# Kernel optimization log

Hardware: AMD Instinct MI355X
Metric: run time of the kernel (lower is better)

Reference implementation:

```python
import jax, jax.numpy as jnp
import numpy as np

B, D = 16384, 1280      # batch, EfficientNet-b0 feature dim (model._fc.in_features)
C1, C2, C3 = 8, 6, 4    # fanout per tree level: 8 roots, 6 children each, 4 leaves each


def setup_inputs() -> dict:
    key = jax.random.key(0)
    ks = jax.random.split(key, 7)
    sc = 0.02
    x = jax.random.normal(ks[0], (B, D), dtype=jnp.float32)
    # root classifier: self.final = Linear(1280 -> n[0]=8)
    W_final = jax.random.normal(ks[1], (D, C1), dtype=jnp.float32) * sc
    b_final = jnp.zeros((C1,), dtype=jnp.float32)
    # level-1 node linears: Linear(1281 -> 6); split into feature part Wp and upper-scalar column wu
    Wp1 = jax.random.normal(ks[2], (C1, D, C2), dtype=jnp.float32) * sc
    wu1 = jax.random.normal(ks[3], (C1, C2), dtype=jnp.float32) * sc
    b1 = jnp.zeros((C1, C2), dtype=jnp.float32)
    # level-2 node linears: Linear(1281 -> 4)
    Wp2 = jax.random.normal(ks[4], (C1, C2, D, C3), dtype=jnp.float32) * sc
    wu2 = jax.random.normal(ks[5], (C1, C2, C3), dtype=jnp.float32) * sc
    b2 = jnp.zeros((C1, C2, C3), dtype=jnp.float32)
    return {"x": x, "W_final": W_final, "b_final": b_final,
            "Wp1": Wp1, "wu1": wu1, "b1": b1,
            "Wp2": Wp2, "wu2": wu2, "b2": b2}


def reference(x, W_final, b_final, Wp1, wu1, b1, Wp2, wu2, b2):
    # penultimate = x.clone().detach()
    pen = jax.lax.stop_gradient(x)                      # (B, D)
    # root: raw final-linear outputs (NO softmax at root in the torch code)
    u1 = x @ W_final + b_final                          # (B, C1) == upper for level-1 nodes
    # level-1 nodes: line = softmax(Linear([pen, upper_scalar]))
    # Linear([pen, u]) == pen @ Wp + u * wu + b  (batched over all 8 nodes in one GEMM)
    logits1 = jnp.einsum('bd,idc->bic', pen, Wp1) + u1[:, :, None] * wu1[None] + b1[None]
    p1 = jax.nn.softmax(logits1, axis=-1)               # (B, C1, C2)
    u2 = p1 * u1[:, :, None]                            # upper for level-2 nodes
    # level-2 nodes
    logits2 = jnp.einsum('bd,ijdc->bijc', pen, Wp2) + u2[..., None] * wu2[None] + b2[None]
    p2 = jax.nn.softmax(logits2, axis=-1)               # (B, C1, C2, C3)
    u3 = p2 * u2[..., None]                             # upper for leaf nodes
    # output: for each node (sorted by path length, then lexicographic path),
    # the last column of xdict[node] == upper[node]. Row-major reshape matches
    # the sorted key order for single-char labels.
    return jnp.concatenate([u1, u2.reshape(B, C1 * C2), u3.reshape(B, C1 * C2 * C3)], axis=1)
```

## Files before the change

kernel.cpp:

```cpp
#include <hip/hip_runtime.h>
#include <stdint.h>
#include <stddef.h>

#define D_FEAT 1280
#define N_PAD  256
#define N_OUT  248
#define BM     32
#define BK     64
#define K_ITERS 20
#define W_TILE_BYTES (N_PAD * BK * 2)

typedef float f32x4 __attribute__((ext_vector_type(4)));
typedef short s16x8 __attribute__((ext_vector_type(8)));
typedef unsigned int u32x4 __attribute__((ext_vector_type(4)));

__device__ __forceinline__ unsigned int cvt_pk(float a, float b) {
  unsigned int r;
  asm("v_cvt_pk_bf16_f32 %0, %1, %2" : "=v"(r) : "v"(a), "v"(b));
  return r;
}

__device__ __forceinline__ void gload16(const void* g, void* l) {
  __builtin_amdgcn_global_load_lds(
      (const __attribute__((address_space(1))) void*)g,
      (__attribute__((address_space(3))) void*)l, 16, 0, 0);
}

__global__ __launch_bounds__(256) void pack_w_kernel(
    const float* __restrict__ Wf, const float* __restrict__ Wp1,
    const float* __restrict__ Wp2, unsigned short* __restrict__ out) {
  int chunk = blockIdx.x * 256 + threadIdx.x;
  int s_phys = chunk & 7;
  int n = (chunk >> 3) & 255;
  int kt = chunk >> 11;
  int s_log = s_phys ^ (n & 7);
  int d0 = kt * BK + s_log * 8;
  float v[8];
#pragma unroll
  for (int e = 0; e < 8; ++e) v[e] = 0.0f;
  if (n < 8) {
#pragma unroll
    for (int e = 0; e < 8; ++e) v[e] = Wf[(d0 + e) * 8 + n];
  } else if (n < 56) {
    int m = n - 8;
    const float* base = Wp1 + (size_t)(m / 6) * D_FEAT * 6 + (m % 6);
#pragma unroll
    for (int e = 0; e < 8; ++e) v[e] = base[(d0 + e) * 6];
  } else if (n < 248) {
    int m = n - 56;
    const float* base = Wp2 + ((size_t)(m / 24) * 6 + ((m % 24) >> 2)) * D_FEAT * 4 + (m & 3);
#pragma unroll
    for (int e = 0; e < 8; ++e) v[e] = base[(d0 + e) * 4];
  }
  union { u32x4 u; s16x8 s; } pk;
#pragma unroll
  for (int h = 0; h < 4; ++h) pk.u[h] = cvt_pk(v[2 * h], v[2 * h + 1]);
  *(s16x8*)(out + (size_t)chunk * 8) = pk.s;
}

__global__ __launch_bounds__(256, 2) void tree_head_kernel(
    const float* __restrict__ x, const unsigned short* __restrict__ Wb,
    const float* __restrict__ b_final, const float* __restrict__ wu1,
    const float* __restrict__ b1, const float* __restrict__ wu2,
    const float* __restrict__ b2, float* __restrict__ out) {
  __shared__ __align__(16) char smem[73728];
  char* Ab0 = smem;
  char* Ab1 = smem + 4096;
  char* Bb0 = smem + 8192;
  char* Bb1 = smem + 40960;

  const int tid  = threadIdx.x;
  const int lane = tid & 63;
  const int wave = tid >> 6;
  const int l15  = lane & 15;
  const int lh   = lane >> 4;
  const int row0 = blockIdx.x * BM;

  f32x4 acc[2][4];
#pragma unroll
  for (int m = 0; m < 2; ++m)
#pragma unroll
    for (int n = 0; n < 4; ++n)
#pragma unroll
      for (int j = 0; j < 4; ++j) acc[m][n][j] = 0.0f;

  const int arow = tid >> 3;
  const int aslot = tid & 7;
  const char* aptr = (const char*)x + ((size_t)(row0 + arow) * D_FEAT + aslot * 8) * 4;
  const int awoff = arow * 128 + ((aslot ^ (arow & 7)) << 4);
  const char* bsrc = (const char*)Wb + wave * 1024 + lane * 16;
  const int bdst = wave * 1024;

  f32x4 ra[3][2];

#define STAGEB(kt_, dB_) do {                                                 \
    _Pragma("unroll")                                                         \
    for (int j_ = 0; j_ < 8; ++j_)                                            \
      gload16(bsrc + (size_t)(kt_) * W_TILE_BYTES + j_ * 4096,                \
              (dB_) + bdst + j_ * 4096);                                      \
  } while (0)

#define LOADA(kt_, ri_) do {                                                  \
    ra[ri_][0] = *(const f32x4*)(aptr + (kt_) * 256);                         \
    ra[ri_][1] = *(const f32x4*)(aptr + (kt_) * 256 + 16);                    \
  } while (0)

#define WRITEA(ri_, dA_) do {                                                 \
    union { u32x4 u; s16x8 s; } pk_;                                          \
    pk_.u[0] = cvt_pk(ra[ri_][0][0], ra[ri_][0][1]);                          \
    pk_.u[1] = cvt_pk(ra[ri_][0][2], ra[ri_][0][3]);                          \
    pk_.u[2] = cvt_pk(ra[ri_][1][0], ra[ri_][1][1]);                          \
    pk_.u[3] = cvt_pk(ra[ri_][1][2], ra[ri_][1][3]);                          \
    *(s16x8*)((dA_) + awoff) = pk_.s;                                         \
  } while (0)

#define COMPUTE(cA_, cB_) do {                                                \
    s16x8 fr[2][2];                                                           \
    _Pragma("unroll")                                                         \
    for (int m_ = 0; m_ < 2; ++m_) {                                          \
      int rl_ = m_ * 16 + l15;                                                \
      _Pragma("unroll")                                                       \
      for (int ks_ = 0; ks_ < 2; ++ks_) {                                     \
        int sl_ = ks_ * 4 + lh;                                               \
        fr[m_][ks_] = *(const s16x8*)((cA_) + rl_ * 128 +                     \
                                      ((sl_ ^ (rl_ & 7)) << 4));              \
      }                                                                       \
    }                                                                         \
    _Pragma("unroll")                                                         \
    for (int ks_ = 0; ks_ < 2; ++ks_) {                                       \
      int sl_ = ks_ * 4 + lh;                                                 \
      _Pragma("unroll")                                                       \
      for (int nf_ = 0; nf_ < 4; ++nf_) {                                     \
        int n_ = wave * 64 + nf_ * 16 + l15;                                  \
        s16x8 b_ = *(const s16x8*)((cB_) + n_ * 128 + ((sl_ ^ (n_ & 7)) << 4));\
        acc[0][nf_] = __builtin_amdgcn_mfma_f32_16x16x32_bf16(fr[0][ks_], b_, acc[0][nf_], 0, 0, 0); \
        acc[1][nf_] = __builtin_amdgcn_mfma_f32_16x16x32_bf16(fr[1][ks_], b_, acc[1][nf_], 0, 0, 0); \
      }                                                                       \
    }                                                                         \
  } while (0)

#define ITER(vm_, cA_, cB_, wA_, sB_, skt_, lakt_, ls_, ws_) do {             \
    asm volatile("s_waitcnt vmcnt(" #vm_ ") lgkmcnt(0)" ::: "memory");        \
    __builtin_amdgcn_sched_barrier(0);                                        \
    __builtin_amdgcn_s_barrier();                                             \
    __builtin_amdgcn_sched_barrier(0);                                        \
    STAGEB(skt_, sB_);                                                        \
    LOADA(lakt_, ls_);                                                        \
    __builtin_amdgcn_sched_barrier(0);                                        \
    WRITEA(ws_, wA_);                                                         \
    COMPUTE(cA_, cB_);                                                        \
  } while (0)

  STAGEB(0, Bb0);
  LOADA(0, 0);
  LOADA(1, 1);
  LOADA(2, 2);
  __builtin_amdgcn_sched_barrier(0);
  asm volatile("s_waitcnt vmcnt(4)" ::: "memory");
  __builtin_amdgcn_sched_barrier(0);
  WRITEA(0, Ab0);

  for (int t = 0; t < 2; ++t) {
    ITER(2, Ab0, Bb0, Ab1, Bb1, 6 * t + 1, 6 * t + 3, 0, 1);
    ITER(2, Ab1, Bb1, Ab0, Bb0, 6 * t + 2, 6 * t + 4, 1, 2);
    ITER(2, Ab0, Bb0, Ab1, Bb1, 6 * t + 3, 6 * t + 5, 2, 0);
    ITER(2, Ab1, Bb1, Ab0, Bb0, 6 * t + 4, 6 * t + 6, 0, 1);
    ITER(2, Ab0, Bb0, Ab1, Bb1, 6 * t + 5, 6 * t + 7, 1, 2);
    ITER(2, Ab1, Bb1, Ab0, Bb0, 6 * t + 6, 6 * t + 8, 2, 0);
  }
  ITER(2, Ab0, Bb0, Ab1, Bb1, 13, 15, 0, 1);
  ITER(2, Ab1, Bb1, Ab0, Bb0, 14, 16, 1, 2);
  ITER(2, Ab0, Bb0, Ab1, Bb1, 15, 17, 2, 0);
  ITER(2, Ab1, Bb1, Ab0, Bb0, 16, 18, 0, 1);
  ITER(2, Ab0, Bb0, Ab1, Bb1, 17, 19, 1, 2);

  asm volatile("s_waitcnt vmcnt(2) lgkmcnt(0)" ::: "memory");
  __builtin_amdgcn_sched_barrier(0);
  __builtin_amdgcn_s_barrier();
  __builtin_amdgcn_sched_barrier(0);
  STAGEB(18, Bb0);
  __builtin_amdgcn_sched_barrier(0);
  WRITEA(0, Ab0);
  COMPUTE(Ab1, Bb1);

  asm volatile("s_waitcnt vmcnt(0) lgkmcnt(0)" ::: "memory");
  __builtin_amdgcn_sched_barrier(0);
  __builtin_amdgcn_s_barrier();
  __builtin_amdgcn_sched_barrier(0);
  STAGEB(19, Bb1);
  __builtin_amdgcn_sched_barrier(0);
  WRITEA(1, Ab1);
  COMPUTE(Ab0, Bb0);

  asm volatile("s_waitcnt vmcnt(0) lgkmcnt(0)" ::: "memory");
  __builtin_amdgcn_sched_barrier(0);
  __builtin_amdgcn_s_barrier();
  __builtin_amdgcn_sched_barrier(0);
  COMPUTE(Ab1, Bb1);

  __syncthreads();

  float* Ls = (float*)smem;
#pragma unroll
  for (int m = 0; m < 2; ++m)
#pragma unroll
    for (int nf = 0; nf < 4; ++nf) {
      int col = wave * 64 + nf * 16 + l15;
      if (col < N_OUT) {
        int rbase = m * 16 + (lh << 2);
#pragma unroll
        for (int i = 0; i < 4; ++i) Ls[col * 33 + rbase + i] = acc[m][nf][i];
      }
    }
  __syncthreads();

  const int p = tid & 7;
  const int r = tid >> 3;
  float* orow = out + (size_t)(row0 + r) * N_OUT;

  float ui = Ls[p * 33 + r] + b_final[p];
  orow[p] = ui;

  float lg[6];
  float mx = -1e30f;
#pragma unroll
  for (int c = 0; c < 6; ++c) {
    lg[c] = Ls[(8 + p * 6 + c) * 33 + r] + ui * wu1[p * 6 + c] + b1[p * 6 + c];
    mx = fmaxf(mx, lg[c]);
  }
  float s = 0.0f;
#pragma unroll
  for (int c = 0; c < 6; ++c) { lg[c] = __expf(lg[c] - mx); s += lg[c]; }
  float sc = ui / s;
  float u2v[6];
#pragma unroll
  for (int c = 0; c < 6; ++c) {
    u2v[c] = lg[c] * sc;
    orow[8 + p * 6 + c] = u2v[c];
  }

#pragma unroll
  for (int j = 0; j < 6; ++j) {
    int g = p * 6 + j;
    float ug = u2v[j];
    float l2[4];
    float m2 = -1e30f;
#pragma unroll
    for (int c = 0; c < 4; ++c) {
      l2[c] = Ls[(56 + g * 4 + c) * 33 + r] + ug * wu2[g * 4 + c] + b2[g * 4 + c];
      m2 = fmaxf(m2, l2[c]);
    }
    float s2 = 0.0f;
#pragma unroll
    for (int c = 0; c < 4; ++c) { l2[c] = __expf(l2[c] - m2); s2 += l2[c]; }
    float sc2 = ug / s2;
    f32x4 o;
#pragma unroll
    for (int c = 0; c < 4; ++c) o[c] = l2[c] * sc2;
    *(f32x4*)(orow + 56 + g * 4) = o;
  }
#undef STAGEB
#undef LOADA
#undef WRITEA
#undef COMPUTE
#undef ITER
}

extern "C" void kernel_launch(void* const* d_in, const int* in_sizes, int n_in,
                              void* d_out, int out_size, void* d_ws, size_t ws_size,
                              hipStream_t stream) {
  const float* x   = (const float*)d_in[0];
  const float* Wf  = (const float*)d_in[1];
  const float* bf  = (const float*)d_in[2];
  const float* Wp1 = (const float*)d_in[3];
  const float* wu1 = (const float*)d_in[4];
  const float* b1  = (const float*)d_in[5];
  const float* Wp2 = (const float*)d_in[6];
  const float* wu2 = (const float*)d_in[7];
  const float* b2  = (const float*)d_in[8];
  float* out = (float*)d_out;
  unsigned short* Wb = (unsigned short*)d_ws;

  pack_w_kernel<<<160, 256, 0, stream>>>(Wf, Wp1, Wp2, Wb);
  tree_head_kernel<<<16384 / BM, 256, 0, stream>>>(x, Wb, bf, wu1, b1, wu2, b2, out);
}
```

Baseline: 37.92 us.

## Load A fragments directly to registers and give each wave private B buffers

```diff
diff --git a/kernel.cpp b/kernel.cpp
--- a/kernel.cpp
+++ b/kernel.cpp
@@ -63,11 +63,7 @@
     const float* __restrict__ b_final, const float* __restrict__ wu1,
     const float* __restrict__ b1, const float* __restrict__ wu2,
     const float* __restrict__ b2, float* __restrict__ out) {
-  __shared__ __align__(16) char smem[73728];
-  char* Ab0 = smem;
-  char* Ab1 = smem + 4096;
-  char* Bb0 = smem + 8192;
-  char* Bb1 = smem + 40960;
+  __shared__ __align__(16) char smem[65536];
 
   const int tid  = threadIdx.x;
   const int lane = tid & 63;
@@ -76,6 +72,8 @@
   const int lh   = lane >> 4;
   const int row0 = blockIdx.x * BM;
 
+  char* Bme = smem + wave * 16384;
+
   f32x4 acc[2][4];
 #pragma unroll
   for (int m = 0; m < 2; ++m)
@@ -84,119 +82,88 @@
 #pragma unroll
       for (int j = 0; j < 4; ++j) acc[m][n][j] = 0.0f;
 
-  const int arow = tid >> 3;
-  const int aslot = tid & 7;
-  const char* aptr = (const char*)x + ((size_t)(row0 + arow) * D_FEAT + aslot * 8) * 4;
-  const int awoff = arow * 128 + ((aslot ^ (arow & 7)) << 4);
-  const char* bsrc = (const char*)Wb + wave * 1024 + lane * 16;
-  const int bdst = wave * 1024;
-
-  f32x4 ra[3][2];
-
-#define STAGEB(kt_, dB_) do {                                                 \
+  const char* abase = (const char*)x
+      + ((size_t)(row0 + l15) * D_FEAT + lh * 8) * 4;
+  const char* bsrc = (const char*)Wb + wave * 8192 + lane * 16;
+
+  f32x4 ra[3][8];
+
+#define STAGEB(kt_, db_) do {                                                 \
     _Pragma("unroll")                                                         \
     for (int j_ = 0; j_ < 8; ++j_)                                            \
-      gload16(bsrc + (size_t)(kt_) * W_TILE_BYTES + j_ * 4096,                \
-              (dB_) + bdst + j_ * 4096);                                      \
-  } while (0)
-
-#define LOADA(kt_, ri_) do {                                                  \
-    ra[ri_][0] = *(const f32x4*)(aptr + (kt_) * 256);                         \
-    ra[ri_][1] = *(const f32x4*)(aptr + (kt_) * 256 + 16);                    \
-  } while (0)
-
-#define WRITEA(ri_, dA_) do {                                                 \
-    union { u32x4 u; s16x8 s; } pk_;                                          \
-    pk_.u[0] = cvt_pk(ra[ri_][0][0], ra[ri_][0][1]);                          \
-    pk_.u[1] = cvt_pk(ra[ri_][0][2], ra[ri_][0][3]);                          \
-    pk_.u[2] = cvt_pk(ra[ri_][1][0], ra[ri_][1][1]);                          \
-    pk_.u[3] = cvt_pk(ra[ri_][1][2], ra[ri_][1][3]);                          \
-    *(s16x8*)((dA_) + awoff) = pk_.s;                                         \
-  } while (0)
-
-#define COMPUTE(cA_, cB_) do {                                                \
+      gload16(bsrc + (size_t)(kt_) * W_TILE_BYTES + j_ * 1024,                \
+              Bme + (db_) * 8192 + j_ * 1024);                                \
+  } while (0)
+
+#define LOADA(kt_, s_) do {                                                   \
+    _Pragma("unroll")                                                         \
+    for (int m_ = 0; m_ < 2; ++m_)                                            \
+      _Pragma("unroll")                                                       \
+      for (int ks_ = 0; ks_ < 2; ++ks_)                                       \
+        _Pragma("unroll")                                                     \
+        for (int h_ = 0; h_ < 2; ++h_)                                        \
+          ra[s_][m_ * 4 + ks_ * 2 + h_] = *(const f32x4*)(                    \
+              abase + m_ * (16 * D_FEAT * 4) + (kt_) * 256 + ks_ * 128 + h_ * 16); \
+  } while (0)
+
+#define COMPUTE(s_, db_) do {                                                 \
     s16x8 fr[2][2];                                                           \
     _Pragma("unroll")                                                         \
-    for (int m_ = 0; m_ < 2; ++m_) {                                          \
-      int rl_ = m_ * 16 + l15;                                                \
+    for (int m_ = 0; m_ < 2; ++m_)                                            \
       _Pragma("unroll")                                                       \
       for (int ks_ = 0; ks_ < 2; ++ks_) {                                     \
-        int sl_ = ks_ * 4 + lh;                                               \
-        fr[m_][ks_] = *(const s16x8*)((cA_) + rl_ * 128 +                     \
-                                      ((sl_ ^ (rl_ & 7)) << 4));              \
+        union { u32x4 u; s16x8 s; } pk_;                                      \
+        f32x4 f0_ = ra[s_][m_ * 4 + ks_ * 2];                                 \
+        f32x4 f1_ = ra[s_][m_ * 4 + ks_ * 2 + 1];                             \
+        pk_.u[0] = cvt_pk(f0_[0], f0_[1]); pk_.u[1] = cvt_pk(f0_[2], f0_[3]); \
+        pk_.u[2] = cvt_pk(f1_[0], f1_[1]); pk_.u[3] = cvt_pk(f1_[2], f1_[3]); \
+        fr[m_][ks_] = pk_.s;                                                  \
       }                                                                       \
-    }                                                                         \
+    __builtin_amdgcn_s_setprio(1);                                            \
     _Pragma("unroll")                                                         \
     for (int ks_ = 0; ks_ < 2; ++ks_) {                                       \
       int sl_ = ks_ * 4 + lh;                                                 \
       _Pragma("unroll")                                                       \
       for (int nf_ = 0; nf_ < 4; ++nf_) {                                     \
-        int n_ = wave * 64 + nf_ * 16 + l15;                                  \
-        s16x8 b_ = *(const s16x8*)((cB_) + n_ * 128 + ((sl_ ^ (n_ & 7)) << 4));\
+        int nl_ = nf_ * 16 + l15;                                             \
+        s16x8 b_ = *(const s16x8*)(Bme + (db_) * 8192 + nl_ * 128 +           \
+                                   ((sl_ ^ (nl_ & 7)) << 4));                 \
         acc[0][nf_] = __builtin_amdgcn_mfma_f32_16x16x32_bf16(fr[0][ks_], b_, acc[0][nf_], 0, 0, 0); \
         acc[1][nf_] = __builtin_amdgcn_mfma_f32_16x16x32_bf16(fr[1][ks_], b_, acc[1][nf_], 0, 0, 0); \
       }                                                                       \
     }                                                                         \
-  } while (0)
-
-#define ITER(vm_, cA_, cB_, wA_, sB_, skt_, lakt_, ls_, ws_) do {             \
-    asm volatile("s_waitcnt vmcnt(" #vm_ ") lgkmcnt(0)" ::: "memory");        \
+    __builtin_amdgcn_s_setprio(0);                                            \
+  } while (0)
+
+#define ITER(kt_, db_, dbn_, sc_, sn_) do {                                   \
+    asm volatile("s_waitcnt vmcnt(8)" ::: "memory");                          \
     __builtin_amdgcn_sched_barrier(0);                                        \
-    __builtin_amdgcn_s_barrier();                                             \
+    STAGEB((kt_) + 1, dbn_);                                                  \
+    LOADA((kt_) + 2, sn_);                                                    \
     __builtin_amdgcn_sched_barrier(0);                                        \
-    STAGEB(skt_, sB_);                                                        \
-    LOADA(lakt_, ls_);                                                        \
-    __builtin_amdgcn_sched_barrier(0);                                        \
-    WRITEA(ws_, wA_);                                                         \
-    COMPUTE(cA_, cB_);                                                        \
-  } while (0)
-
-  STAGEB(0, Bb0);
+    COMPUTE(sc_, db_);                                                        \
+  } while (0)
+
+  STAGEB(0, 0);
   LOADA(0, 0);
   LOADA(1, 1);
-  LOADA(2, 2);
+
+  for (int t = 0; t < 3; ++t) {
+    ITER(6 * t + 0, 0, 1, 0, 2);
+    ITER(6 * t + 1, 1, 0, 1, 0);
+    ITER(6 * t + 2, 0, 1, 2, 1);
+    ITER(6 * t + 3, 1, 0, 0, 2);
+    ITER(6 * t + 4, 0, 1, 1, 0);
+    ITER(6 * t + 5, 1, 0, 2, 1);
+  }
+  asm volatile("s_waitcnt vmcnt(8)" ::: "memory");
   __builtin_amdgcn_sched_barrier(0);
-  asm volatile("s_waitcnt vmcnt(4)" ::: "memory");
+  STAGEB(19, 1);
   __builtin_amdgcn_sched_barrier(0);
-  WRITEA(0, Ab0);
-
-  for (int t = 0; t < 2; ++t) {
-    ITER(2, Ab0, Bb0, Ab1, Bb1, 6 * t + 1, 6 * t + 3, 0, 1);
-    ITER(2, Ab1, Bb1, Ab0, Bb0, 6 * t + 2, 6 * t + 4, 1, 2);
-    ITER(2, Ab0, Bb0, Ab1, Bb1, 6 * t + 3, 6 * t + 5, 2, 0);
-    ITER(2, Ab1, Bb1, Ab0, Bb0, 6 * t + 4, 6 * t + 6, 0, 1);
-    ITER(2, Ab0, Bb0, Ab1, Bb1, 6 * t + 5, 6 * t + 7, 1, 2);
-    ITER(2, Ab1, Bb1, Ab0, Bb0, 6 * t + 6, 6 * t + 8, 2, 0);
-  }
-  ITER(2, Ab0, Bb0, Ab1, Bb1, 13, 15, 0, 1);
-  ITER(2, Ab1, Bb1, Ab0, Bb0, 14, 16, 1, 2);
-  ITER(2, Ab0, Bb0, Ab1, Bb1, 15, 17, 2, 0);
-  ITER(2, Ab1, Bb1, Ab0, Bb0, 16, 18, 0, 1);
-  ITER(2, Ab0, Bb0, Ab1, Bb1, 17, 19, 1, 2);
-
-  asm volatile("s_waitcnt vmcnt(2) lgkmcnt(0)" ::: "memory");
+  COMPUTE(0, 0);
+  asm volatile("s_waitcnt vmcnt(0)" ::: "memory");
   __builtin_amdgcn_sched_barrier(0);
-  __builtin_amdgcn_s_barrier();
-  __builtin_amdgcn_sched_barrier(0);
-  STAGEB(18, Bb0);
-  __builtin_amdgcn_sched_barrier(0);
-  WRITEA(0, Ab0);
-  COMPUTE(Ab1, Bb1);
-
-  asm volatile("s_waitcnt vmcnt(0) lgkmcnt(0)" ::: "memory");
-  __builtin_amdgcn_sched_barrier(0);
-  __builtin_amdgcn_s_barrier();
-  __builtin_amdgcn_sched_barrier(0);
-  STAGEB(19, Bb1);
-  __builtin_amdgcn_sched_barrier(0);
-  WRITEA(1, Ab1);
-  COMPUTE(Ab0, Bb0);
-
-  asm volatile("s_waitcnt vmcnt(0) lgkmcnt(0)" ::: "memory");
-  __builtin_amdgcn_sched_barrier(0);
-  __builtin_amdgcn_s_barrier();
-  __builtin_amdgcn_sched_barrier(0);
-  COMPUTE(Ab1, Bb1);
+  COMPUTE(1, 1);
 
   __syncthreads();
 
@@ -261,7 +228,6 @@
   }
 #undef STAGEB
 #undef LOADA
-#undef WRITEA
 #undef COMPUTE
 #undef ITER
 }
```

New measurement: 61.26 us. 1.62x slower.

## Double row tile to 64 with 8 waves sharing each weight tile

Applied to the files above, without the earlier changes.

```diff
diff --git a/kernel.cpp b/kernel.cpp
--- a/kernel.cpp
+++ b/kernel.cpp
@@ -5,7 +5,7 @@
 #define D_FEAT 1280
 #define N_PAD  256
 #define N_OUT  248
-#define BM     32
+#define BM     64
 #define BK     64
 #define K_ITERS 20
 #define W_TILE_BYTES (N_PAD * BK * 2)
@@ -58,20 +58,22 @@
   *(s16x8*)(out + (size_t)chunk * 8) = pk.s;
 }
 
-__global__ __launch_bounds__(256, 2) void tree_head_kernel(
+__global__ __launch_bounds__(512, 4) void tree_head_kernel(
     const float* __restrict__ x, const unsigned short* __restrict__ Wb,
     const float* __restrict__ b_final, const float* __restrict__ wu1,
     const float* __restrict__ b1, const float* __restrict__ wu2,
     const float* __restrict__ b2, float* __restrict__ out) {
-  __shared__ __align__(16) char smem[73728];
+  __shared__ __align__(16) char smem[81920];
   char* Ab0 = smem;
-  char* Ab1 = smem + 4096;
-  char* Bb0 = smem + 8192;
-  char* Bb1 = smem + 40960;
+  char* Ab1 = smem + 8192;
+  char* Bb0 = smem + 16384;
+  char* Bb1 = smem + 49152;
 
   const int tid  = threadIdx.x;
   const int lane = tid & 63;
   const int wave = tid >> 6;
+  const int wm   = wave >> 2;
+  const int wn   = wave & 3;
   const int l15  = lane & 15;
   const int lh   = lane >> 4;
   const int row0 = blockIdx.x * BM;
@@ -95,9 +97,9 @@
 
 #define STAGEB(kt_, dB_) do {                                                 \
     _Pragma("unroll")                                                         \
-    for (int j_ = 0; j_ < 8; ++j_)                                            \
-      gload16(bsrc + (size_t)(kt_) * W_TILE_BYTES + j_ * 4096,                \
-              (dB_) + bdst + j_ * 4096);                                      \
+    for (int j_ = 0; j_ < 4; ++j_)                                            \
+      gload16(bsrc + (size_t)(kt_) * W_TILE_BYTES + j_ * 8192,                \
+              (dB_) + bdst + j_ * 8192);                                      \
   } while (0)
 
 #define LOADA(kt_, ri_) do {                                                  \
@@ -118,7 +120,7 @@
     s16x8 fr[2][2];                                                           \
     _Pragma("unroll")                                                         \
     for (int m_ = 0; m_ < 2; ++m_) {                                          \
-      int rl_ = m_ * 16 + l15;                                                \
+      int rl_ = wm * 32 + m_ * 16 + l15;                                      \
       _Pragma("unroll")                                                       \
       for (int ks_ = 0; ks_ < 2; ++ks_) {                                     \
         int sl_ = ks_ * 4 + lh;                                               \
@@ -131,7 +133,7 @@
       int sl_ = ks_ * 4 + lh;                                                 \
       _Pragma("unroll")                                                       \
       for (int nf_ = 0; nf_ < 4; ++nf_) {                                     \
-        int n_ = wave * 64 + nf_ * 16 + l15;                                  \
+        int n_ = wn * 64 + nf_ * 16 + l15;                                    \
         s16x8 b_ = *(const s16x8*)((cB_) + n_ * 128 + ((sl_ ^ (n_ & 7)) << 4));\
         acc[0][nf_] = __builtin_amdgcn_mfma_f32_16x16x32_bf16(fr[0][ks_], b_, acc[0][nf_], 0, 0, 0); \
         acc[1][nf_] = __builtin_amdgcn_mfma_f32_16x16x32_bf16(fr[1][ks_], b_, acc[1][nf_], 0, 0, 0); \
@@ -139,57 +141,57 @@
     }                                                                         \
   } while (0)
 
-#define ITER(vm_, cA_, cB_, wA_, sB_, skt_, lakt_, ls_, ws_) do {             \
-    asm volatile("s_waitcnt vmcnt(" #vm_ ") lgkmcnt(0)" ::: "memory");        \
+#define ITER(cA_, cB_, wA_, sB_, skt_, lakt_, ls_, ws_) do {                  \
+    asm volatile("s_waitcnt vmcnt(2) lgkmcnt(0)" ::: "memory");               \
     __builtin_amdgcn_sched_barrier(0);                                        \
     __builtin_amdgcn_s_barrier();                                             \
     __builtin_amdgcn_sched_barrier(0);                                        \
+    WRITEA(ws_, wA_);                                                         \
     STAGEB(skt_, sB_);                                                        \
     LOADA(lakt_, ls_);                                                        \
     __builtin_amdgcn_sched_barrier(0);                                        \
-    WRITEA(ws_, wA_);                                                         \
     COMPUTE(cA_, cB_);                                                        \
   } while (0)
 
-  STAGEB(0, Bb0);
   LOADA(0, 0);
   LOADA(1, 1);
+  STAGEB(0, Bb0);
   LOADA(2, 2);
   __builtin_amdgcn_sched_barrier(0);
-  asm volatile("s_waitcnt vmcnt(4)" ::: "memory");
+  asm volatile("s_waitcnt vmcnt(8)" ::: "memory");
   __builtin_amdgcn_sched_barrier(0);
   WRITEA(0, Ab0);
 
   for (int t = 0; t < 2; ++t) {
-    ITER(2, Ab0, Bb0, Ab1, Bb1, 6 * t + 1, 6 * t + 3, 0, 1);
-    ITER(2, Ab1, Bb1, Ab0, Bb0, 6 * t + 2, 6 * t + 4, 1, 2);
-    ITER(2, Ab0, Bb0, Ab1, Bb1, 6 * t + 3, 6 * t + 5, 2, 0);
-    ITER(2, Ab1, Bb1, Ab0, Bb0, 6 * t + 4, 6 * t + 6, 0, 1);
-    ITER(2, Ab0, Bb0, Ab1, Bb1, 6 * t + 5, 6 * t + 7, 1, 2);
-    ITER(2, Ab1, Bb1, Ab0, Bb0, 6 * t + 6, 6 * t + 8, 2, 0);
-  }
-  ITER(2, Ab0, Bb0, Ab1, Bb1, 13, 15, 0, 1);
-  ITER(2, Ab1, Bb1, Ab0, Bb0, 14, 16, 1, 2);
-  ITER(2, Ab0, Bb0, Ab1, Bb1, 15, 17, 2, 0);
-  ITER(2, Ab1, Bb1, Ab0, Bb0, 16, 18, 0, 1);
-  ITER(2, Ab0, Bb0, Ab1, Bb1, 17, 19, 1, 2);
+    ITER(Ab0, Bb0, Ab1, Bb1, 6 * t + 1, 6 * t + 3, 0, 1);
+    ITER(Ab1, Bb1, Ab0, Bb0, 6 * t + 2, 6 * t + 4, 1, 2);
+    ITER(Ab0, Bb0, Ab1, Bb1, 6 * t + 3, 6 * t + 5, 2, 0);
+    ITER(Ab1, Bb1, Ab0, Bb0, 6 * t + 4, 6 * t + 6, 0, 1);
+    ITER(Ab0, Bb0, Ab1, Bb1, 6 * t + 5, 6 * t + 7, 1, 2);
+    ITER(Ab1, Bb1, Ab0, Bb0, 6 * t + 6, 6 * t + 8, 2, 0);
+  }
+  ITER(Ab0, Bb0, Ab1, Bb1, 13, 15, 0, 1);
+  ITER(Ab1, Bb1, Ab0, Bb0, 14, 16, 1, 2);
+  ITER(Ab0, Bb0, Ab1, Bb1, 15, 17, 2, 0);
+  ITER(Ab1, Bb1, Ab0, Bb0, 16, 18, 0, 1);
+  ITER(Ab0, Bb0, Ab1, Bb1, 17, 19, 1, 2);
 
   asm volatile("s_waitcnt vmcnt(2) lgkmcnt(0)" ::: "memory");
   __builtin_amdgcn_sched_barrier(0);
   __builtin_amdgcn_s_barrier();
   __builtin_amdgcn_sched_barrier(0);
+  WRITEA(0, Ab0);
   STAGEB(18, Bb0);
   __builtin_amdgcn_sched_barrier(0);
-  WRITEA(0, Ab0);
   COMPUTE(Ab1, Bb1);
 
   asm volatile("s_waitcnt vmcnt(0) lgkmcnt(0)" ::: "memory");
   __builtin_amdgcn_sched_barrier(0);
   __builtin_amdgcn_s_barrier();
   __builtin_amdgcn_sched_barrier(0);
+  WRITEA(1, Ab1);
   STAGEB(19, Bb1);
   __builtin_amdgcn_sched_barrier(0);
-  WRITEA(1, Ab1);
   COMPUTE(Ab0, Bb0);
 
   asm volatile("s_waitcnt vmcnt(0) lgkmcnt(0)" ::: "memory");
@@ -205,11 +207,11 @@
   for (int m = 0; m < 2; ++m)
 #pragma unroll
     for (int nf = 0; nf < 4; ++nf) {
-      int col = wave * 64 + nf * 16 + l15;
+      int col = wn * 64 + nf * 16 + l15;
       if (col < N_OUT) {
-        int rbase = m * 16 + (lh << 2);
-#pragma unroll
-        for (int i = 0; i < 4; ++i) Ls[col * 33 + rbase + i] = acc[m][nf][i];
+        int rbase = wm * 32 + m * 16 + (lh << 2);
+#pragma unroll
+        for (int i = 0; i < 4; ++i) Ls[col * 65 + rbase + i] = acc[m][nf][i];
       }
     }
   __syncthreads();
@@ -218,14 +220,14 @@
   const int r = tid >> 3;
   float* orow = out + (size_t)(row0 + r) * N_OUT;
 
-  float ui = Ls[p * 33 + r] + b_final[p];
+  float ui = Ls[p * 65 + r] + b_final[p];
   orow[p] = ui;
 
   float lg[6];
   float mx = -1e30f;
 #pragma unroll
   for (int c = 0; c < 6; ++c) {
-    lg[c] = Ls[(8 + p * 6 + c) * 33 + r] + ui * wu1[p * 6 + c] + b1[p * 6 + c];
+    lg[c] = Ls[(8 + p * 6 + c) * 65 + r] + ui * wu1[p * 6 + c] + b1[p * 6 + c];
     mx = fmaxf(mx, lg[c]);
   }
   float s = 0.0f;
@@ -247,7 +249,7 @@
     float m2 = -1e30f;
 #pragma unroll
     for (int c = 0; c < 4; ++c) {
-      l2[c] = Ls[(56 + g * 4 + c) * 33 + r] + ug * wu2[g * 4 + c] + b2[g * 4 + c];
+      l2[c] = Ls[(56 + g * 4 + c) * 65 + r] + ug * wu2[g * 4 + c] + b2[g * 4 + c];
       m2 = fmaxf(m2, l2[c]);
     }
     float s2 = 0.0f;
@@ -282,5 +284,5 @@
   unsigned short* Wb = (unsigned short*)d_ws;
 
   pack_w_kernel<<<160, 256, 0, stream>>>(Wf, Wp1, Wp2, Wb);
-  tree_head_kernel<<<16384 / BM, 256, 0, stream>>>(x, Wb, bf, wu1, b1, wu2, b2, out);
-}
+  tree_head_kernel<<<16384 / BM, 512, 0, stream>>>(x, Wb, bf, wu1, b1, wu2, b2, out);
+}
```

Result: no change. 37.36 us (-1.5%).
